# Performance work log

Hardware: AMD Instinct MI355X
Metric: run time of the kernel (lower is better)

The kernel has to match this reference:

```python
import jax, jax.numpy as jnp
import numpy as np

G = 72  # landmark groups
HID = 64  # hidden per landmark
FEAT = 288  # cnn features per landmark (32 ch * 3*3 spatial)


def _conv(x, w, b):
    # grouped valid conv, NCHW / OIHW
    y = jax.lax.conv_general_dilated(
        x, w, window_strides=(1, 1), padding='VALID',
        dimension_numbers=('NCHW', 'OIHW', 'NCHW'), feature_group_count=G)
    return y + b[None, :, None, None]


def _maxpool2(x):
    return jax.lax.reduce_window(x, -jnp.inf, jax.lax.max,
                                 (1, 1, 2, 2), (1, 1, 2, 2), 'VALID')


def setup_inputs() -> dict:
    key = jax.random.key(0)
    ks = jax.random.split(key, 10)
    s = 0.02
    inp = {
        'x': jax.random.normal(ks[0], (64, 216, 46, 46), jnp.float32),
        # conv1: 3*72 -> 8*72, k=5, groups=72 => in/group = 3
        'w1': jax.random.normal(ks[1], (576, 3, 5, 5), jnp.float32) * s,
        'b1': jax.random.normal(ks[2], (576,), jnp.float32) * s,
        # conv2: 8*72 -> 16*72, k=3
        'w2': jax.random.normal(ks[3], (1152, 8, 3, 3), jnp.float32) * s,
        'b2': jax.random.normal(ks[4], (1152,), jnp.float32) * s,
        # conv3: 16*72 -> 32*72, k=3
        'w3': jax.random.normal(ks[5], (2304, 16, 3, 3), jnp.float32) * s,
        'b3': jax.random.normal(ks[6], (2304,), jnp.float32) * s,
        # linear1: 20736 -> 4608, no bias (masked block-diagonal)
        'lin1_w': jax.random.normal(ks[7], (4608, 20736), jnp.float32) * s,
        # linear2: 4608 -> 144, with bias (masked block-diagonal)
        'lin2_w': jax.random.normal(ks[8], (144, 4608), jnp.float32) * s,
        'lin2_b': jax.random.normal(ks[9], (144,), jnp.float32) * s,
    }
    return inp


def reference(x, w1, b1, w2, b2, w3, b3, lin1_w, lin2_w, lin2_b):
    # CNN stack: (conv -> relu -> maxpool) x3
    h = _maxpool2(jax.nn.relu(_conv(x, w1, b1)))   # (B,576,21,21)
    h = _maxpool2(jax.nn.relu(_conv(h, w2, b2)))   # (B,1152,9,9)
    h = _maxpool2(jax.nn.relu(_conv(h, w3, b3)))   # (B,2304,3,3)
    B = h.shape[0]
    h = h.reshape(B, -1)  # (B, 20736), channel-major flatten like torch.flatten(x,-3)

    eye = jnp.eye(G, dtype=h.dtype)
    # mask1: (20736, 4608); mask1.T multiplies linear1.weight (4608,20736)
    m1 = jnp.repeat(jnp.repeat(eye, HID, axis=1), FEAT, axis=0)
    out = h @ (lin1_w * m1.T).T  # (B, 4608)
    # mask2: (4608, 144)
    m2 = jnp.repeat(jnp.repeat(eye, 2, axis=1), HID, axis=0)
    out = out @ (lin2_w * m2.T).T + lin2_b  # (B, 144)
    return out
```

## Files before the change

### kernel.cpp

```cpp
#include <hip/hip_runtime.h>

#define NG 72

typedef _Float16 half2f __attribute__((ext_vector_type(2)));

__device__ __forceinline__ unsigned pkrtz(float a, float b) {
  return __builtin_bit_cast(unsigned, __builtin_amdgcn_cvt_pkrtz(a, b));
}
__device__ __forceinline__ float dot2(unsigned win, unsigned wgt, float acc) {
  return __builtin_amdgcn_fdot2(__builtin_bit_cast(half2f, win),
                                __builtin_bit_cast(half2f, wgt), acc, false);
}

#define WIN(E, O, r, c) (((c) & 1) ? (O)[(r)][(c) >> 1] : (E)[(r)][(c) >> 1])

#define H1S 444
#define H2S 84

__global__ __launch_bounds__(256) void prep_k(const float* __restrict__ w1,
                                              const float* __restrict__ w2,
                                              const float* __restrict__ w3,
                                              unsigned* __restrict__ wf) {
  const int i = blockIdx.x * 256 + threadIdx.x;
  if (i < 28800) {
    const int t = i % 25, p = (i / 25) & 1, ocg = i / 50;
    const float* base = w1 + (size_t)ocg * 75 + t;
    const float a = base[p * 50];
    const float b = (p == 0) ? base[25] : 0.f;
    wf[i] = pkrtz(a, b);
  } else if (i < 70272) {
    const int j = i - 28800;
    const int t = j % 9, p = (j / 9) & 3, ocg = j / 36;
    const float* base = w2 + (size_t)ocg * 72 + t;
    wf[i] = pkrtz(base[2 * p * 9], base[(2 * p + 1) * 9]);
  } else if (i < 236160) {
    const int j = i - 70272;
    const int t = j % 9, p = (j / 9) & 7, ocg = j / 72;
    const float* base = w3 + (size_t)ocg * 144 + t;
    wf[i] = pkrtz(base[2 * p * 9], base[(2 * p + 1) * 9]);
  }
}

__global__ __launch_bounds__(448) void conv1_k(const float* __restrict__ x,
                                               const unsigned* __restrict__ wf,
                                               const float* __restrict__ bias,
                                               float* __restrict__ out) {
  const int b = blockIdx.x / NG, g = blockIdx.x % NG;
  __shared__ unsigned sxe[2][46][26];
  __shared__ unsigned sxo[2][46][26];
  const float* xp = x + (size_t)(b * 216 + g * 3) * 2116;
  const float4* q0 = (const float4*)xp;
  const float4* q1 = (const float4*)(xp + 2116);
  const float4* q2 = (const float4*)(xp + 2 * 2116);
  for (int i = threadIdx.x; i < 529; i += 448) {
    const float4 a = q0[i], c1 = q1[i], c2 = q2[i];
#pragma unroll
    for (int j = 0; j < 4; j++) {
      const int k = 4 * i + j, r = k / 46, cc = k % 46;
      const unsigned v0 = pkrtz((&a.x)[j], (&c1.x)[j]);
      const unsigned v1 = pkrtz((&c2.x)[j], 0.f);
      if (cc & 1) { sxo[0][r][cc >> 1] = v0; sxo[1][r][cc >> 1] = v1; }
      else        { sxe[0][r][cc >> 1] = v0; sxe[1][r][cc >> 1] = v1; }
    }
  }
  __syncthreads();
  const unsigned* wgq = wf + (size_t)(g * 8) * 50;
  const float* bg = bias + g * 8;
  const int tid = threadIdx.x;
  if (tid < 441) {
    const int yl = tid / 21, px = tid % 21;
    const int iy = 2 * yl;
    float acc[8][4];
#pragma unroll
    for (int o = 0; o < 8; o++)
#pragma unroll
      for (int q = 0; q < 4; q++) acc[o][q] = 0.f;
#pragma unroll 1
    for (int p = 0; p < 2; p++) {
      unsigned we[6][3], wo[6][3];
#pragma unroll
      for (int r = 0; r < 6; r++)
#pragma unroll
        for (int j = 0; j < 3; j++) {
          we[r][j] = sxe[p][iy + r][px + j];
          wo[r][j] = sxo[p][iy + r][px + j];
        }
#pragma unroll
      for (int oc = 0; oc < 8; oc++) {
        const unsigned* wq = wgq + (oc * 2 + p) * 25;
#pragma unroll
        for (int ky = 0; ky < 5; ky++)
#pragma unroll
          for (int kx = 0; kx < 5; kx++) {
            const unsigned wv = wq[ky * 5 + kx];
            acc[oc][0] = dot2(WIN(we, wo, ky,     kx),     wv, acc[oc][0]);
            acc[oc][1] = dot2(WIN(we, wo, ky,     kx + 1), wv, acc[oc][1]);
            acc[oc][2] = dot2(WIN(we, wo, ky + 1, kx),     wv, acc[oc][2]);
            acc[oc][3] = dot2(WIN(we, wo, ky + 1, kx + 1), wv, acc[oc][3]);
          }
      }
    }
#pragma unroll
    for (int oc = 0; oc < 8; oc++) {
      const float v = fmaxf(fmaxf(acc[oc][0], acc[oc][1]), fmaxf(acc[oc][2], acc[oc][3])) + bg[oc];
      out[(size_t)(b * 576 + g * 8 + oc) * H1S + yl * 21 + px] = fmaxf(v, 0.f);
    }
  }
}

#define C2_NBB 3
__global__ __launch_bounds__(256) void conv2_k(const float* __restrict__ x,
                                               const unsigned* __restrict__ wf,
                                               const float* __restrict__ bias,
                                               float* __restrict__ out) {
  const int g = blockIdx.x % NG, b0 = (blockIdx.x / NG) * C2_NBB;
  const int nbb = min(C2_NBB, 64 - b0);
  __shared__ unsigned sxp[C2_NBB][4][21][22];
  for (int bb = 0; bb < nbb; bb++) {
    const float* xp = x + (size_t)((b0 + bb) * 576 + g * 8) * H1S;
    for (int i = threadIdx.x; i < 4 * 111; i += 256) {
      const int p = i / 111, i4 = i % 111;
      const float4 a  = *(const float4*)(xp + (2 * p) * H1S + 4 * i4);
      const float4 b4 = *(const float4*)(xp + (2 * p + 1) * H1S + 4 * i4);
#pragma unroll
      for (int j = 0; j < 4; j++) {
        const int e = 4 * i4 + j;
        if (e < 441) sxp[bb][p][e / 21][e % 21] = pkrtz((&a.x)[j], (&b4.x)[j]);
      }
    }
  }
  __syncthreads();
  const unsigned* wg = wf + (size_t)(g * 16) * 36;
  const float* bg = bias + g * 16;
  for (int u = threadIdx.x; u < nbb * 81; u += 256) {
    const int bb = u / 81, pp = u % 81, py = pp / 9, px = pp % 9;
    const int iy = 2 * py, ix = 2 * px;
    float acc[16][4];
#pragma unroll
    for (int o = 0; o < 16; o++)
#pragma unroll
      for (int q = 0; q < 4; q++) acc[o][q] = 0.f;
#pragma unroll 1
    for (int p = 0; p < 4; p++) {
      unsigned winp[4][4];
#pragma unroll
      for (int r = 0; r < 4; r++)
#pragma unroll
        for (int c = 0; c < 4; c++) winp[r][c] = sxp[bb][p][iy + r][ix + c];
#pragma unroll
      for (int oc = 0; oc < 16; oc++) {
        const unsigned* wq = wg + (oc * 4 + p) * 9;
#pragma unroll
        for (int ky = 0; ky < 3; ky++)
#pragma unroll
          for (int kx = 0; kx < 3; kx++) {
            const unsigned wv = wq[ky * 3 + kx];
            acc[oc][0] = dot2(winp[ky][kx],         wv, acc[oc][0]);
            acc[oc][1] = dot2(winp[ky][kx + 1],     wv, acc[oc][1]);
            acc[oc][2] = dot2(winp[ky + 1][kx],     wv, acc[oc][2]);
            acc[oc][3] = dot2(winp[ky + 1][kx + 1], wv, acc[oc][3]);
          }
      }
    }
#pragma unroll
    for (int oc = 0; oc < 16; oc++) {
      const float v = fmaxf(fmaxf(acc[oc][0], acc[oc][1]), fmaxf(acc[oc][2], acc[oc][3])) + bg[oc];
      out[(size_t)((b0 + bb) * 1152 + g * 16 + oc) * H2S + pp] = fmaxf(v, 0.f);
    }
  }
}

#define C3_NBB 7
__global__ __launch_bounds__(256) void conv3_k(const float* __restrict__ x,
                                               const unsigned* __restrict__ wf,
                                               const float* __restrict__ bias,
                                               float* __restrict__ out) {
  const int g = blockIdx.x % NG, b0 = (blockIdx.x / NG) * C3_NBB;
  const int nbb = min(C3_NBB, 64 - b0);
  __shared__ unsigned sxp[C3_NBB][8][9][10];
  for (int bb = 0; bb < nbb; bb++) {
    const float* xp = x + (size_t)((b0 + bb) * 1152 + g * 16) * H2S;
    for (int i = threadIdx.x; i < 8 * 21; i += 256) {
      const int p = i / 21, i4 = i % 21;
      const float4 a  = *(const float4*)(xp + (2 * p) * H2S + 4 * i4);
      const float4 b4 = *(const float4*)(xp + (2 * p + 1) * H2S + 4 * i4);
#pragma unroll
      for (int j = 0; j < 4; j++) {
        const int e = 4 * i4 + j;
        if (e < 81) sxp[bb][p][e / 9][e % 9] = pkrtz((&a.x)[j], (&b4.x)[j]);
      }
    }
  }
  __syncthreads();
  const int ocg = __builtin_amdgcn_readfirstlane(threadIdx.x >> 6);
  const unsigned* wg = wf + ((size_t)(g * 32 + ocg * 8)) * 72;
  const float* bg = bias + g * 32 + ocg * 8;
  const int lane = threadIdx.x & 63;
  const int bb = lane / 9, pp = lane % 9;
  if (bb < nbb) {
    const int py = pp / 3, px = pp % 3, iy = 2 * py, ix = 2 * px;
    float acc[8][4];
#pragma unroll
    for (int o = 0; o < 8; o++)
#pragma unroll
      for (int q = 0; q < 4; q++) acc[o][q] = 0.f;
#pragma unroll 1
    for (int p = 0; p < 8; p++) {
      unsigned winp[4][4];
#pragma unroll
      for (int r = 0; r < 4; r++)
#pragma unroll
        for (int c = 0; c < 4; c++) winp[r][c] = sxp[bb][p][iy + r][ix + c];
#pragma unroll
      for (int o8 = 0; o8 < 8; o8++) {
        const unsigned* wq = wg + (o8 * 8 + p) * 9;
#pragma unroll
        for (int ky = 0; ky < 3; ky++)
#pragma unroll
          for (int kx = 0; kx < 3; kx++) {
            const unsigned wv = wq[ky * 3 + kx];
            acc[o8][0] = dot2(winp[ky][kx],         wv, acc[o8][0]);
            acc[o8][1] = dot2(winp[ky][kx + 1],     wv, acc[o8][1]);
            acc[o8][2] = dot2(winp[ky + 1][kx],     wv, acc[o8][2]);
            acc[o8][3] = dot2(winp[ky + 1][kx + 1], wv, acc[o8][3]);
          }
      }
    }
#pragma unroll
    for (int o8 = 0; o8 < 8; o8++) {
      const float v = fmaxf(fmaxf(acc[o8][0], acc[o8][1]), fmaxf(acc[o8][2], acc[o8][3])) + bg[o8];
      out[(size_t)((b0 + bb) * 2304 + g * 32 + ocg * 8 + o8) * 9 + pp] = fmaxf(v, 0.f);
    }
  }
}

__global__ __launch_bounds__(256) void lin_k(const float* __restrict__ h,
                                             const float* __restrict__ w1,
                                             const float* __restrict__ w2,
                                             const float* __restrict__ b2,
                                             float* __restrict__ out) {
  const int g = blockIdx.x % NG, b0 = (blockIdx.x / NG) * 32;
  __shared__ float sw1[64 * 292];
  __shared__ float sf[32 * 300];
  __shared__ float so[32 * 65];
  __shared__ float sw2[2 * 64];
  __shared__ float sb2[2];
  for (int i = threadIdx.x; i < 64 * 288; i += 256) {
    const int o = i / 288, k = i % 288;
    sw1[o * 292 + k] = w1[(size_t)(g * 64 + o) * 20736 + g * 288 + k];
  }
  for (int i = threadIdx.x; i < 32 * 288; i += 256) {
    const int bb = i / 288, k = i % 288;
    sf[bb * 300 + k] = h[(size_t)(b0 + bb) * 20736 + g * 288 + k];
  }
  if (threadIdx.x < 128) {
    const int j = threadIdx.x >> 6, o = threadIdx.x & 63;
    sw2[j * 64 + o] = w2[(size_t)(g * 2 + j) * 4608 + g * 64 + o];
  }
  if (threadIdx.x < 2) sb2[threadIdx.x] = b2[g * 2 + threadIdx.x];
  __syncthreads();
  const int bp = threadIdx.x & 15, oq = threadIdx.x >> 4;
  const int o0 = 4 * oq;
  float acc[2][4];
#pragma unroll
  for (int i = 0; i < 2; i++)
#pragma unroll
    for (int j = 0; j < 4; j++) acc[i][j] = 0.f;
  for (int k4 = 0; k4 < 72; k4++) {
    const float4 f0 = *(const float4*)&sf[bp * 300 + 4 * k4];
    const float4 f1 = *(const float4*)&sf[(bp + 16) * 300 + 4 * k4];
#pragma unroll
    for (int j = 0; j < 4; j++) {
      const float4 wr = *(const float4*)&sw1[(o0 + j) * 292 + 4 * k4];
      acc[0][j] = fmaf(f0.x, wr.x, fmaf(f0.y, wr.y, fmaf(f0.z, wr.z, fmaf(f0.w, wr.w, acc[0][j]))));
      acc[1][j] = fmaf(f1.x, wr.x, fmaf(f1.y, wr.y, fmaf(f1.z, wr.z, fmaf(f1.w, wr.w, acc[1][j]))));
    }
  }
#pragma unroll
  for (int j = 0; j < 4; j++) {
    so[bp * 65 + o0 + j] = acc[0][j];
    so[(bp + 16) * 65 + o0 + j] = acc[1][j];
  }
  __syncthreads();
  if (threadIdx.x < 64) {
    const int bb = threadIdx.x >> 1, j = threadIdx.x & 1;
    float a = sb2[j];
#pragma unroll 8
    for (int o = 0; o < 64; o++) a = fmaf(so[bb * 65 + o], sw2[j * 64 + o], a);
    out[(b0 + bb) * 144 + g * 2 + j] = a;
  }
}

extern "C" void kernel_launch(void* const* d_in, const int* in_sizes, int n_in,
                              void* d_out, int out_size, void* d_ws, size_t ws_size,
                              hipStream_t stream) {
  const float* x   = (const float*)d_in[0];
  const float* w1  = (const float*)d_in[1];
  const float* b1  = (const float*)d_in[2];
  const float* w2  = (const float*)d_in[3];
  const float* b2  = (const float*)d_in[4];
  const float* w3  = (const float*)d_in[5];
  const float* b3  = (const float*)d_in[6];
  const float* l1w = (const float*)d_in[7];
  const float* l2w = (const float*)d_in[8];
  const float* l2b = (const float*)d_in[9];
  float* out = (float*)d_out;

  float* h1 = (float*)d_ws;
  float* h2 = h1 + 16367616;
  float* h3 = h2 + 6193152;
  unsigned* wf = (unsigned*)(h3 + 1327104);

  prep_k <<<dim3(923),     256, 0, stream>>>(w1, w2, w3, wf);
  conv1_k<<<dim3(64 * NG), 448, 0, stream>>>(x,  wf,         b1, h1);
  conv2_k<<<dim3(22 * NG), 256, 0, stream>>>(h1, wf + 28800, b2, h2);
  conv3_k<<<dim3(10 * NG), 256, 0, stream>>>(h2, wf + 70272, b3, h3);
  lin_k  <<<dim3(2 * NG),  256, 0, stream>>>(h3, l1w, l2w, l2b, out);
}
```

Baseline: 203.0 us.

## Process four batches per conv1 block with register-prefetched input tiles

Each conv1 block now handles four consecutive batch images for one group, with a quarter as many blocks. The next image's input is loaded into registers while the current one is being computed, so global load latency overlaps with the dot2 compute and weight loads are amortised across four images. In exchange there are fewer blocks (1152) and more registers per thread, which may lower occupancy and parallelism on the device.

```diff
diff --git a/kernel.cpp b/kernel.cpp
--- a/kernel.cpp
+++ b/kernel.cpp
@@ -45,65 +45,96 @@
                                                const unsigned* __restrict__ wf,
                                                const float* __restrict__ bias,
                                                float* __restrict__ out) {
-  const int b = blockIdx.x / NG, g = blockIdx.x % NG;
+  const int g = blockIdx.x % NG, bq = blockIdx.x / NG;
   __shared__ unsigned sxe[2][46][26];
   __shared__ unsigned sxo[2][46][26];
-  const float* xp = x + (size_t)(b * 216 + g * 3) * 2116;
-  const float4* q0 = (const float4*)xp;
-  const float4* q1 = (const float4*)(xp + 2116);
-  const float4* q2 = (const float4*)(xp + 2 * 2116);
-  for (int i = threadIdx.x; i < 529; i += 448) {
-    const float4 a = q0[i], c1 = q1[i], c2 = q2[i];
-#pragma unroll
-    for (int j = 0; j < 4; j++) {
-      const int k = 4 * i + j, r = k / 46, cc = k % 46;
-      const unsigned v0 = pkrtz((&a.x)[j], (&c1.x)[j]);
-      const unsigned v1 = pkrtz((&c2.x)[j], 0.f);
-      if (cc & 1) { sxo[0][r][cc >> 1] = v0; sxo[1][r][cc >> 1] = v1; }
-      else        { sxe[0][r][cc >> 1] = v0; sxe[1][r][cc >> 1] = v1; }
-    }
-  }
-  __syncthreads();
   const unsigned* wgq = wf + (size_t)(g * 8) * 50;
   const float* bg = bias + g * 8;
   const int tid = threadIdx.x;
-  if (tid < 441) {
-    const int yl = tid / 21, px = tid % 21;
-    const int iy = 2 * yl;
-    float acc[8][4];
-#pragma unroll
-    for (int o = 0; o < 8; o++)
-#pragma unroll
-      for (int q = 0; q < 4; q++) acc[o][q] = 0.f;
+  const int i0 = tid, i1 = tid + 448;
+  const float* xp0 = x + ((size_t)(bq * 4) * 216 + g * 3) * 2116;
+  float4 rA0 = ((const float4*)xp0)[i0];
+  float4 rA1 = ((const float4*)(xp0 + 2116))[i0];
+  float4 rA2 = ((const float4*)(xp0 + 2 * 2116))[i0];
+  float4 rB0, rB1, rB2;
+  if (tid < 81) {
+    rB0 = ((const float4*)xp0)[i1];
+    rB1 = ((const float4*)(xp0 + 2116))[i1];
+    rB2 = ((const float4*)(xp0 + 2 * 2116))[i1];
+  }
 #pragma unroll 1
-    for (int p = 0; p < 2; p++) {
-      unsigned we[6][3], wo[6][3];
-#pragma unroll
-      for (int r = 0; r < 6; r++)
-#pragma unroll
-        for (int j = 0; j < 3; j++) {
-          we[r][j] = sxe[p][iy + r][px + j];
-          wo[r][j] = sxo[p][iy + r][px + j];
+  for (int t = 0; t < 4; t++) {
+    __syncthreads();
+#pragma unroll
+    for (int j = 0; j < 4; j++) {
+      const int k = 4 * i0 + j, r = k / 46, cc = k % 46;
+      const unsigned v0 = pkrtz((&rA0.x)[j], (&rA1.x)[j]);
+      const unsigned v1 = pkrtz((&rA2.x)[j], 0.f);
+      if (cc & 1) { sxo[0][r][cc >> 1] = v0; sxo[1][r][cc >> 1] = v1; }
+      else        { sxe[0][r][cc >> 1] = v0; sxe[1][r][cc >> 1] = v1; }
+    }
+    if (tid < 81) {
+#pragma unroll
+      for (int j = 0; j < 4; j++) {
+        const int k = 4 * i1 + j, r = k / 46, cc = k % 46;
+        const unsigned v0 = pkrtz((&rB0.x)[j], (&rB1.x)[j]);
+        const unsigned v1 = pkrtz((&rB2.x)[j], 0.f);
+        if (cc & 1) { sxo[0][r][cc >> 1] = v0; sxo[1][r][cc >> 1] = v1; }
+        else        { sxe[0][r][cc >> 1] = v0; sxe[1][r][cc >> 1] = v1; }
+      }
+    }
+    __syncthreads();
+    if (t < 3) {
+      const float* xp = x + ((size_t)(bq * 4 + t + 1) * 216 + g * 3) * 2116;
+      rA0 = ((const float4*)xp)[i0];
+      rA1 = ((const float4*)(xp + 2116))[i0];
+      rA2 = ((const float4*)(xp + 2 * 2116))[i0];
+      if (tid < 81) {
+        rB0 = ((const float4*)xp)[i1];
+        rB1 = ((const float4*)(xp + 2116))[i1];
+        rB2 = ((const float4*)(xp + 2 * 2116))[i1];
+      }
+    }
+    if (tid < 441) {
+      const int b = bq * 4 + t;
+      const int yl = tid / 21, px = tid % 21;
+      const int iy = 2 * yl;
+      float acc[8][4];
+#pragma unroll
+      for (int o = 0; o < 8; o++)
+#pragma unroll
+        for (int q = 0; q < 4; q++) acc[o][q] = 0.f;
+#pragma unroll 1
+      for (int p = 0; p < 2; p++) {
+        unsigned we[6][3], wo[6][3];
+#pragma unroll
+        for (int r = 0; r < 6; r++)
+#pragma unroll
+          for (int j = 0; j < 3; j++) {
+            we[r][j] = sxe[p][iy + r][px + j];
+            wo[r][j] = sxo[p][iy + r][px + j];
+          }
+#pragma unroll
+        for (int oc = 0; oc < 8; oc++) {
+          const unsigned* wq = wgq + (oc * 2 + p) * 25;
+#pragma unroll
+          for (int ky = 0; ky < 5; ky++)
+#pragma unroll
+            for (int kx = 0; kx < 5; kx++) {
+              const unsigned wv = wq[ky * 5 + kx];
+              acc[oc][0] = dot2(WIN(we, wo, ky,     kx),     wv, acc[oc][0]);
+              acc[oc][1] = dot2(WIN(we, wo, ky,     kx + 1), wv, acc[oc][1]);
+              acc[oc][2] = dot2(WIN(we, wo, ky + 1, kx),     wv, acc[oc][2]);
+              acc[oc][3] = dot2(WIN(we, wo, ky + 1, kx + 1), wv, acc[oc][3]);
+            }
         }
+      }
 #pragma unroll
       for (int oc = 0; oc < 8; oc++) {
-        const unsigned* wq = wgq + (oc * 2 + p) * 25;
-#pragma unroll
-        for (int ky = 0; ky < 5; ky++)
-#pragma unroll
-          for (int kx = 0; kx < 5; kx++) {
-            const unsigned wv = wq[ky * 5 + kx];
-            acc[oc][0] = dot2(WIN(we, wo, ky,     kx),     wv, acc[oc][0]);
-            acc[oc][1] = dot2(WIN(we, wo, ky,     kx + 1), wv, acc[oc][1]);
-            acc[oc][2] = dot2(WIN(we, wo, ky + 1, kx),     wv, acc[oc][2]);
-            acc[oc][3] = dot2(WIN(we, wo, ky + 1, kx + 1), wv, acc[oc][3]);
-          }
-      }
-    }
-#pragma unroll
-    for (int oc = 0; oc < 8; oc++) {
-      const float v = fmaxf(fmaxf(acc[oc][0], acc[oc][1]), fmaxf(acc[oc][2], acc[oc][3])) + bg[oc];
-      out[(size_t)(b * 576 + g * 8 + oc) * H1S + yl * 21 + px] = fmaxf(v, 0.f);
+        const float v = fmaxf(fmaxf(acc[oc][0], acc[oc][1]),
+                              fmaxf(acc[oc][2], acc[oc][3])) + bg[oc];
+        out[(size_t)(b * 576 + g * 8 + oc) * H1S + yl * 21 + px] = fmaxf(v, 0.f);
+      }
     }
   }
 }
@@ -312,7 +343,7 @@
   unsigned* wf = (unsigned*)(h3 + 1327104);
 
   prep_k <<<dim3(923),     256, 0, stream>>>(w1, w2, w3, wf);
-  conv1_k<<<dim3(64 * NG), 448, 0, stream>>>(x,  wf,         b1, h1);
+  conv1_k<<<dim3(16 * NG), 448, 0, stream>>>(x,  wf,         b1, h1);
   conv2_k<<<dim3(22 * NG), 256, 0, stream>>>(h1, wf + 28800, b2, h2);
   conv3_k<<<dim3(10 * NG), 256, 0, stream>>>(h2, wf + 70272, b3, h3);
   lin_k  <<<dim3(2 * NG),  256, 0, stream>>>(h3, l1w, l2w, l2b, out);
```

New measurement: 216.6 us. 1.07x slower.
